# Kernel optimization log

Measured on AMD Instinct MI355X. Metric: run time of the kernel, lower is better.

## Reference

```python
import jax, jax.numpy as jnp
import numpy as np

N_NODES = 100000
N_EDGES = 3200000
NODE_DIM = 16      # output_size_node
EDGE_IN = 2 * NODE_DIM  # input_size_Edge = 32
EDGE_OUT = 9
HIDDEN = 9
MSG_ROUNDS = 3


def _mlp_params(key, d_in, d_hid, d_out):
    k1, k2, k3 = jax.random.split(key, 3)
    s1 = 1.0 / np.sqrt(d_in)
    s2 = 1.0 / np.sqrt(d_hid)
    return (
        jax.random.normal(k1, (d_in, d_hid), jnp.float32) * s1,
        jnp.zeros((d_hid,), jnp.float32),
        jax.random.normal(k2, (d_hid, d_hid), jnp.float32) * s2,
        jnp.zeros((d_hid,), jnp.float32),
        jax.random.normal(k3, (d_hid, d_out), jnp.float32) * s2,
        jnp.zeros((d_out,), jnp.float32),
    )


def setup_inputs() -> dict:
    key = jax.random.key(0)
    kx, ks, kd, kfe, kfx = jax.random.split(key, 5)
    X = jax.random.normal(kx, (N_NODES, NODE_DIM), jnp.float32)
    edge_src = jax.random.randint(ks, (N_EDGES,), 0, N_NODES, jnp.int32)
    edge_dst = jax.random.randint(kd, (N_EDGES,), 0, N_NODES, jnp.int32)
    fe = _mlp_params(kfe, EDGE_IN, HIDDEN, EDGE_OUT)
    fx = _mlp_params(kfx, EDGE_OUT + NODE_DIM, HIDDEN, NODE_DIM)
    return {
        "X": X, "edge_src": edge_src, "edge_dst": edge_dst,
        "fe_W1": fe[0], "fe_b1": fe[1], "fe_W2": fe[2], "fe_b2": fe[3], "fe_W3": fe[4], "fe_b3": fe[5],
        "fx_W1": fx[0], "fx_b1": fx[1], "fx_W2": fx[2], "fx_b2": fx[3], "fx_W3": fx[4], "fx_b3": fx[5],
    }


def _mlp3(h, W1, b1, W2, b2, W3, b3):
    # 3-layer MLP with relu hidden activations (MLP_nonlinear, act='relu')
    h = jax.nn.relu(h @ W1 + b1)
    h = jax.nn.relu(h @ W2 + b2)
    return h @ W3 + b3


def reference(X, edge_src, edge_dst,
              fe_W1, fe_b1, fe_W2, fe_b2, fe_W3, fe_b3,
              fx_W1, fx_b1, fx_W2, fx_b2, fx_W3, fx_b3):
    n = X.shape[0]
    for _ in range(MSG_ROUNDS):
        # per-edge message: fe(cat(X[i], X[j])) with i=receiver(dst), j=sender(src)
        e_in = jnp.concatenate([X[edge_dst], X[edge_src]], axis=-1)  # [E, 2*D]
        msgs = _mlp3(e_in, fe_W1, fe_b1, fe_W2, fe_b2, fe_W3, fe_b3)  # [E, 9]
        m = jax.ops.segment_sum(msgs, edge_dst, num_segments=n)       # [N, 9]
        # per-node update: fx(cat(X[i], m_i))
        X = _mlp3(jnp.concatenate([X, m], axis=-1),
                  fx_W1, fx_b1, fx_W2, fx_b2, fx_W3, fx_b3)           # [N, D]
    return X
```

## Files before the change

### kernel.cpp

```cpp
#include <hip/hip_runtime.h>


constexpr int NN = 100000;
constexpr int NE = 3200000;
constexpr int NBK = (NN + 127) / 128;
constexpr int SLOT = 8192;
constexpr int EPB = 4096;
constexpr int NBLK_SORT = (NE + EPB - 1) / EPB;
constexpr int NB_NODE = (NN + 255) / 256;


__global__ __launch_bounds__(256) void bsort_k(const int* __restrict__ src,
                                               const int* __restrict__ dst,
                                               int* __restrict__ gcursor,
                                               unsigned* __restrict__ sed)
{
    __shared__ int lhist[NBK];
    __shared__ int lbase[NBK];
    const int t = threadIdx.x;
    for (int i = t; i < NBK; i += 256) lhist[i] = 0;
    __syncthreads();

    const int blkbase = blockIdx.x * EPB;
    unsigned pr[16], sv[16];
    #pragma unroll
    for (int k = 0; k < 16; ++k) {
        const int e = blkbase + k * 256 + t;
        if (e < NE) {
            const int d = dst[e];
            const int s = src[e];
            const int bin = d >> 7;
            const int r = atomicAdd(&lhist[bin], 1);
            pr[k] = ((unsigned)bin << 13) | (unsigned)r;
            sv[k] = ((unsigned)(d & 127) << 17) | (unsigned)s;
        } else {
            pr[k] = 0xFFFFFFFFu;
        }
    }
    __syncthreads();

    for (int i = t; i < NBK; i += 256) {
        const int c = lhist[i];
        if (c) lbase[i] = atomicAdd(&gcursor[i], c);
    }
    __syncthreads();

    #pragma unroll
    for (int k = 0; k < 16; ++k) {
        if (pr[k] != 0xFFFFFFFFu) {
            const int bin = (int)(pr[k] >> 13);
            const int r = (int)(pr[k] & 0x1FFFu);
            sed[(size_t)bin * SLOT + lbase[bin] + r] = sv[k];
        }
    }
}


__global__ __launch_bounds__(512) void lsort_k(unsigned* __restrict__ sed,
                                               const int* __restrict__ gcursor)
{
    __shared__ unsigned buf[SLOT];
    __shared__ unsigned obuf[SLOT];
    __shared__ int hist[128];
    __shared__ int cur[128];
    const int t = threadIdx.x;
    const int b = blockIdx.x;
    const int base = b * SLOT;
    int fill = gcursor[b];
    if (fill > SLOT) fill = SLOT;

    if (t < 128) hist[t] = 0;
    __syncthreads();
    for (int i = t; i < fill; i += 512) {
        unsigned v = sed[base + i];
        buf[i] = v;
        atomicAdd(&hist[v >> 17], 1);
    }
    __syncthreads();
    if (t < 128) cur[t] = hist[t];
    __syncthreads();
    for (int off = 1; off < 128; off <<= 1) {
        int a = (t < 128 && t >= off) ? cur[t - off] : 0;
        __syncthreads();
        if (t < 128) cur[t] += a;
        __syncthreads();
    }
    if (t < 128) cur[t] -= hist[t];
    __syncthreads();
    for (int i = t; i < fill; i += 512) {
        unsigned v = buf[i];
        int r = atomicAdd(&cur[v >> 17], 1);
        obuf[r] = v;
    }
    __syncthreads();
    for (int i = t; i < fill; i += 512) sed[base + i] = obuf[i];
}


__global__ __launch_bounds__(256) void base_k(const float* __restrict__ X,
                                              const float* __restrict__ feW1,
                                              const float* __restrict__ feb1,
                                              float* __restrict__ base1,
                                              float* __restrict__ bases,
                                              float* __restrict__ m)
{
    const int n = blockIdx.x * 256 + threadIdx.x;
    if (n >= NN) return;

    float x[16];
    const float4* p = reinterpret_cast<const float4*>(X + (size_t)n * 16);
    #pragma unroll
    for (int q = 0; q < 4; ++q) {
        float4 v = p[q];
        x[4*q] = v.x; x[4*q+1] = v.y; x[4*q+2] = v.z; x[4*q+3] = v.w;
    }
    float bd[9];
    #pragma unroll
    for (int j = 0; j < 9; ++j) bd[j] = feb1[j];
    #pragma unroll
    for (int i = 0; i < 16; ++i) {
        const float xi = x[i];
        #pragma unroll
        for (int j = 0; j < 9; ++j) bd[j] = fmaf(xi, feW1[i * 9 + j], bd[j]);
    }
    float bs[9];
    #pragma unroll
    for (int j = 0; j < 9; ++j) bs[j] = 0.f;
    #pragma unroll
    for (int i = 0; i < 16; ++i) {
        const float xi = x[i];
        #pragma unroll
        for (int j = 0; j < 9; ++j) bs[j] = fmaf(xi, feW1[(16 + i) * 9 + j], bs[j]);
    }
    float* bp = base1 + (size_t)n * 12;
    #pragma unroll
    for (int j = 0; j < 9; ++j) bp[j] = bd[j];
    float* sp = bases + (size_t)n * 16;
    #pragma unroll
    for (int j = 0; j < 9; ++j) sp[j] = bs[j];
    float* mp = m + (size_t)n * 10;
    #pragma unroll
    for (int j = 0; j < 10; ++j) mp[j] = 0.f;
}


__global__ __launch_bounds__(256) void edge9_k(
    const float* __restrict__ base1,
    const float* __restrict__ bases,
    const unsigned* __restrict__ sed,
    const int* __restrict__ gcursor,
    const float* __restrict__ feW2, const float* __restrict__ feb2,
    float* __restrict__ m)
{
    const int t = threadIdx.x;
    const int b = blockIdx.x >> 5;
    const int idx0 = (blockIdx.x & 31) * 256;
    const int fill = gcursor[b];
    if (idx0 >= fill) return;

    const int idx = idx0 + t;
    const bool valid = idx < fill;
    const int lane = t & 63;
    const int cidx = valid ? idx : fill - 1;
    const unsigned pk = sed[(size_t)b * SLOT + cidx];
    const int dla = (int)(pk >> 17);
    const int s   = (int)(pk & 0x1FFFFu);
    const int dl  = valid ? dla : 128 + lane;

    float a[9];
    {
        const float4* pb = reinterpret_cast<const float4*>(base1 + (size_t)(b * 128 + dla) * 12);
        float4 b0 = pb[0], b1 = pb[1];
        const float b8 = base1[(size_t)(b * 128 + dla) * 12 + 8];
        const float4* ps = reinterpret_cast<const float4*>(bases + (size_t)s * 16);
        float4 c0 = ps[0], c1 = ps[1];
        const float c8 = bases[(size_t)s * 16 + 8];
        a[0] = b0.x + c0.x; a[1] = b0.y + c0.y; a[2] = b0.z + c0.z; a[3] = b0.w + c0.w;
        a[4] = b1.x + c1.x; a[5] = b1.y + c1.y; a[6] = b1.z + c1.z; a[7] = b1.w + c1.w;
        a[8] = b8 + c8;
    }
    #pragma unroll
    for (int j = 0; j < 9; ++j) a[j] = fmaxf(a[j], 0.f);

    float o[9];
    #pragma unroll
    for (int j = 0; j < 9; ++j) o[j] = feb2[j];
    #pragma unroll
    for (int i = 0; i < 9; ++i) {
        const float ai = a[i];
        #pragma unroll
        for (int j = 0; j < 9; ++j) o[j] = fmaf(ai, feW2[i * 9 + j], o[j]);
    }
    #pragma unroll
    for (int j = 0; j < 9; ++j) o[j] = fmaxf(o[j], 0.f);

    const int dprev = __shfl_up(dl, 1);
    const bool head = (lane == 0) || (dprev != dl);
    const unsigned long long hm = __ballot(head);
    const int dist = __clzll((long long)(hm << (63 - lane)));
    #pragma unroll
    for (int off = 1; off < 64; off <<= 1) {
        const bool ok = (dist >= off);
        #pragma unroll
        for (int j = 0; j < 9; ++j) {
            const float ov = __shfl_up(o[j], off);
            o[j] += ok ? ov : 0.f;
        }
    }
    const bool tail = (lane == 63) || (((hm >> (lane + 1)) & 1ull) != 0ull);
    if (tail && valid) {
        float* mp = m + (size_t)(b * 128 + dl) * 10;
        #pragma unroll
        for (int j = 0; j < 9; ++j) atomicAdd(mp + j, o[j]);
        atomicAdd(mp + 9, (float)(dist + 1));
    }
}


__global__ __launch_bounds__(256) void node8_k(
    const float* __restrict__ Xin, float* __restrict__ m,
    const float* __restrict__ fxW1, const float* __restrict__ fxb1,
    const float* __restrict__ fxW2, const float* __restrict__ fxb2,
    const float* __restrict__ fxW3, const float* __restrict__ fxb3,
    const float* __restrict__ feW1, const float* __restrict__ feb1,
    const float* __restrict__ feW3, const float* __restrict__ feb3,
    float* __restrict__ Xout, float* __restrict__ base1out,
    float* __restrict__ basesout)
{
    const int n = blockIdx.x * 256 + threadIdx.x;
    if (n >= NN) return;

    float xr[16];
    {
        const float4* p = reinterpret_cast<const float4*>(Xin + (size_t)n * 16);
        #pragma unroll
        for (int q = 0; q < 4; ++q) {
            float4 v = p[q];
            xr[4*q] = v.x; xr[4*q+1] = v.y; xr[4*q+2] = v.z; xr[4*q+3] = v.w;
        }
    }
    float S[9], deg;
    float* mp = m + (size_t)n * 10;
    #pragma unroll
    for (int j = 0; j < 9; ++j) S[j] = mp[j];
    deg = mp[9];
    #pragma unroll
    for (int j = 0; j < 10; ++j) mp[j] = 0.f;

    float mm[9];
    #pragma unroll
    for (int j = 0; j < 9; ++j) mm[j] = deg * feb3[j];
    #pragma unroll
    for (int i = 0; i < 9; ++i) {
        const float si = S[i];
        #pragma unroll
        for (int j = 0; j < 9; ++j) mm[j] = fmaf(si, feW3[i * 9 + j], mm[j]);
    }

    float h1[9];
    #pragma unroll
    for (int j = 0; j < 9; ++j) h1[j] = fxb1[j];
    #pragma unroll
    for (int i = 0; i < 16; ++i) {
        const float xi = xr[i];
        #pragma unroll
        for (int j = 0; j < 9; ++j) h1[j] = fmaf(xi, fxW1[i * 9 + j], h1[j]);
    }
    #pragma unroll
    for (int i = 0; i < 9; ++i) {
        const float xi = mm[i];
        #pragma unroll
        for (int j = 0; j < 9; ++j) h1[j] = fmaf(xi, fxW1[(16 + i) * 9 + j], h1[j]);
    }
    #pragma unroll
    for (int j = 0; j < 9; ++j) h1[j] = fmaxf(h1[j], 0.f);

    float h2[9];
    #pragma unroll
    for (int j = 0; j < 9; ++j) h2[j] = fxb2[j];
    #pragma unroll
    for (int i = 0; i < 9; ++i) {
        const float xi = h1[i];
        #pragma unroll
        for (int j = 0; j < 9; ++j) h2[j] = fmaf(xi, fxW2[i * 9 + j], h2[j]);
    }
    #pragma unroll
    for (int j = 0; j < 9; ++j) h2[j] = fmaxf(h2[j], 0.f);

    float o[16];
    #pragma unroll
    for (int k = 0; k < 16; ++k) o[k] = fxb3[k];
    #pragma unroll
    for (int j = 0; j < 9; ++j) {
        const float hj = h2[j];
        #pragma unroll
        for (int k = 0; k < 16; ++k) o[k] = fmaf(hj, fxW3[j * 16 + k], o[k]);
    }

    float4* po = reinterpret_cast<float4*>(Xout + (size_t)n * 16);
    #pragma unroll
    for (int q = 0; q < 4; ++q) {
        float4 v;
        v.x = o[4*q]; v.y = o[4*q+1]; v.z = o[4*q+2]; v.w = o[4*q+3];
        po[q] = v;
    }

    float bb[9];
    #pragma unroll
    for (int j = 0; j < 9; ++j) bb[j] = feb1[j];
    #pragma unroll
    for (int i = 0; i < 16; ++i) {
        const float xi = o[i];
        #pragma unroll
        for (int j = 0; j < 9; ++j) bb[j] = fmaf(xi, feW1[i * 9 + j], bb[j]);
    }
    float* bp = base1out + (size_t)n * 12;
    #pragma unroll
    for (int j = 0; j < 9; ++j) bp[j] = bb[j];

    float cc[9];
    #pragma unroll
    for (int j = 0; j < 9; ++j) cc[j] = 0.f;
    #pragma unroll
    for (int i = 0; i < 16; ++i) {
        const float xi = o[i];
        #pragma unroll
        for (int j = 0; j < 9; ++j) cc[j] = fmaf(xi, feW1[(16 + i) * 9 + j], cc[j]);
    }
    float* sp = basesout + (size_t)n * 16;
    #pragma unroll
    for (int j = 0; j < 9; ++j) sp[j] = cc[j];
}

extern "C" void kernel_launch(void* const* d_in, const int* in_sizes, int n_in,
                              void* d_out, int out_size, void* d_ws, size_t ws_size,
                              hipStream_t stream)
{
    (void)in_sizes; (void)n_in; (void)out_size; (void)ws_size;
    const float* X0   = (const float*)d_in[0];
    const int*   esrc = (const int*)d_in[1];
    const int*   edst = (const int*)d_in[2];
    const float* feW1 = (const float*)d_in[3];
    const float* feb1 = (const float*)d_in[4];
    const float* feW2 = (const float*)d_in[5];
    const float* feb2 = (const float*)d_in[6];
    const float* feW3 = (const float*)d_in[7];
    const float* feb3 = (const float*)d_in[8];
    const float* fxW1 = (const float*)d_in[9];
    const float* fxb1 = (const float*)d_in[10];
    const float* fxW2 = (const float*)d_in[11];
    const float* fxb2 = (const float*)d_in[12];
    const float* fxW3 = (const float*)d_in[13];
    const float* fxb3 = (const float*)d_in[14];
    float* out = (float*)d_out;

    float* base1  = (float*)d_ws;
    float* bases  = base1 + (size_t)NN * 12;
    float* mb     = bases + (size_t)NN * 16;
    int* gcursor  = (int*)(mb + (size_t)NN * 10);
    unsigned* sed = (unsigned*)(gcursor + 1024);

    const dim3 thr(256);
    const dim3 gS(NBLK_SORT);
    const dim3 gL(NBK);
    const dim3 gE(NBK * (SLOT / 256));
    const dim3 gN(NB_NODE);

    hipMemsetAsync(gcursor, 0, NBK * sizeof(int), stream);
    bsort_k<<<gS, thr, 0, stream>>>(esrc, edst, gcursor, sed);
    lsort_k<<<gL, dim3(512), 0, stream>>>(sed, gcursor);

    base_k<<<gN, thr, 0, stream>>>(X0, feW1, feb1, base1, bases, mb);
    edge9_k<<<gE, thr, 0, stream>>>(base1, bases, sed, gcursor, feW2, feb2, mb);
    node8_k<<<gN, thr, 0, stream>>>(X0, mb, fxW1, fxb1, fxW2, fxb2, fxW3, fxb3,
                                    feW1, feb1, feW3, feb3, out, base1, bases);
    edge9_k<<<gE, thr, 0, stream>>>(base1, bases, sed, gcursor, feW2, feb2, mb);
    node8_k<<<gN, thr, 0, stream>>>(out, mb, fxW1, fxb1, fxW2, fxb2, fxW3, fxb3,
                                    feW1, feb1, feW3, feb3, out, base1, bases);
    edge9_k<<<gE, thr, 0, stream>>>(base1, bases, sed, gcursor, feW2, feb2, mb);
    node8_k<<<gN, thr, 0, stream>>>(out, mb, fxW1, fxb1, fxW2, fxb2, fxW3, fxb3,
                                    feW1, feb1, feW3, feb3, out, base1, bases);
}
```

Measured before the change: 492.4 us.

## Process two sorted edges per thread in edge kernel with paired segmented scan

The edge kernel now has each thread handle two consecutive sorted edges, loaded as one uint2. The two messages are pre-combined when they share a destination, and a single segmented warp scan runs over the pairs, with the count carried as a tenth channel. This halves the number of threads and the shuffle-scan work per edge and widens the index loads, at the cost of more registers per thread and more complex head/tail atomic logic. Out-of-range source indices are clamped so padding slots can be read safely.

```diff
diff --git a/kernel.cpp b/kernel.cpp
--- a/kernel.cpp
+++ b/kernel.cpp
@@ -144,7 +144,7 @@
 }
 
 
-__global__ __launch_bounds__(256) void edge9_k(
+__global__ __launch_bounds__(256) void edge11_k(
     const float* __restrict__ base1,
     const float* __restrict__ bases,
     const unsigned* __restrict__ sed,
@@ -153,66 +153,114 @@
     float* __restrict__ m)
 {
     const int t = threadIdx.x;
-    const int b = blockIdx.x >> 5;
-    const int idx0 = (blockIdx.x & 31) * 256;
+    const int b = blockIdx.x >> 4;
+    const int idx0 = (blockIdx.x & 15) * 512;
     const int fill = gcursor[b];
     if (idx0 >= fill) return;
 
-    const int idx = idx0 + t;
-    const bool valid = idx < fill;
     const int lane = t & 63;
-    const int cidx = valid ? idx : fill - 1;
-    const unsigned pk = sed[(size_t)b * SLOT + cidx];
-    const int dla = (int)(pk >> 17);
-    const int s   = (int)(pk & 0x1FFFFu);
-    const int dl  = valid ? dla : 128 + lane;
-
-    float a[9];
+    const int start = idx0 + (t >> 6) * 128;
+    if (start >= fill) return;
+
+    const int e0 = start + 2 * lane;
+    const bool v0 = e0 < fill;
+    const bool v1 = e0 + 1 < fill;
+
+    const uint2 pk = *reinterpret_cast<const uint2*>(sed + (size_t)b * SLOT + e0);
+    const int d0 = (int)(pk.x >> 17);
+    const int d1 = (int)(pk.y >> 17);
+    int s0 = (int)(pk.x & 0x1FFFFu);  s0 = s0 < NN ? s0 : NN - 1;
+    int s1 = (int)(pk.y & 0x1FFFFu);  s1 = s1 < NN ? s1 : NN - 1;
+    const int k0 = v0 ? d0 : (160 + 2 * lane);
+    const int k1 = v1 ? d1 : (161 + 2 * lane);
+
+    float o0[9], o1[9];
     {
-        const float4* pb = reinterpret_cast<const float4*>(base1 + (size_t)(b * 128 + dla) * 12);
+        const float4* pb = reinterpret_cast<const float4*>(base1 + (size_t)(b * 128 + d0) * 12);
         float4 b0 = pb[0], b1 = pb[1];
-        const float b8 = base1[(size_t)(b * 128 + dla) * 12 + 8];
-        const float4* ps = reinterpret_cast<const float4*>(bases + (size_t)s * 16);
+        const float b8 = base1[(size_t)(b * 128 + d0) * 12 + 8];
+        const float4* ps = reinterpret_cast<const float4*>(bases + (size_t)s0 * 16);
         float4 c0 = ps[0], c1 = ps[1];
-        const float c8 = bases[(size_t)s * 16 + 8];
+        const float c8 = bases[(size_t)s0 * 16 + 8];
+        float a[9];
         a[0] = b0.x + c0.x; a[1] = b0.y + c0.y; a[2] = b0.z + c0.z; a[3] = b0.w + c0.w;
         a[4] = b1.x + c1.x; a[5] = b1.y + c1.y; a[6] = b1.z + c1.z; a[7] = b1.w + c1.w;
         a[8] = b8 + c8;
-    }
-    #pragma unroll
-    for (int j = 0; j < 9; ++j) a[j] = fmaxf(a[j], 0.f);
-
-    float o[9];
-    #pragma unroll
-    for (int j = 0; j < 9; ++j) o[j] = feb2[j];
-    #pragma unroll
-    for (int i = 0; i < 9; ++i) {
-        const float ai = a[i];
-        #pragma unroll
-        for (int j = 0; j < 9; ++j) o[j] = fmaf(ai, feW2[i * 9 + j], o[j]);
-    }
-    #pragma unroll
-    for (int j = 0; j < 9; ++j) o[j] = fmaxf(o[j], 0.f);
-
-    const int dprev = __shfl_up(dl, 1);
-    const bool head = (lane == 0) || (dprev != dl);
+        #pragma unroll
+        for (int j = 0; j < 9; ++j) a[j] = fmaxf(a[j], 0.f);
+        #pragma unroll
+        for (int j = 0; j < 9; ++j) o0[j] = feb2[j];
+        #pragma unroll
+        for (int i = 0; i < 9; ++i) {
+            const float ai = a[i];
+            #pragma unroll
+            for (int j = 0; j < 9; ++j) o0[j] = fmaf(ai, feW2[i * 9 + j], o0[j]);
+        }
+        #pragma unroll
+        for (int j = 0; j < 9; ++j) o0[j] = fmaxf(o0[j], 0.f);
+    }
+    {
+        const float4* pb = reinterpret_cast<const float4*>(base1 + (size_t)(b * 128 + d1) * 12);
+        float4 b0 = pb[0], b1 = pb[1];
+        const float b8 = base1[(size_t)(b * 128 + d1) * 12 + 8];
+        const float4* ps = reinterpret_cast<const float4*>(bases + (size_t)s1 * 16);
+        float4 c0 = ps[0], c1 = ps[1];
+        const float c8 = bases[(size_t)s1 * 16 + 8];
+        float a[9];
+        a[0] = b0.x + c0.x; a[1] = b0.y + c0.y; a[2] = b0.z + c0.z; a[3] = b0.w + c0.w;
+        a[4] = b1.x + c1.x; a[5] = b1.y + c1.y; a[6] = b1.z + c1.z; a[7] = b1.w + c1.w;
+        a[8] = b8 + c8;
+        #pragma unroll
+        for (int j = 0; j < 9; ++j) a[j] = fmaxf(a[j], 0.f);
+        #pragma unroll
+        for (int j = 0; j < 9; ++j) o1[j] = feb2[j];
+        #pragma unroll
+        for (int i = 0; i < 9; ++i) {
+            const float ai = a[i];
+            #pragma unroll
+            for (int j = 0; j < 9; ++j) o1[j] = fmaf(ai, feW2[i * 9 + j], o1[j]);
+        }
+        #pragma unroll
+        for (int j = 0; j < 9; ++j) o1[j] = fmaxf(o1[j], 0.f);
+    }
+
+    const bool same = (k0 == k1);
+    float S[10];
+    #pragma unroll
+    for (int j = 0; j < 9; ++j) S[j] = same ? (o0[j] + o1[j]) : o1[j];
+    S[9] = same ? 2.f : (v1 ? 1.f : 0.f);
+
+    const int pkey = __shfl_up(k1, 1);
+    const bool head = (lane == 0) || (pkey != k1);
     const unsigned long long hm = __ballot(head);
     const int dist = __clzll((long long)(hm << (63 - lane)));
     #pragma unroll
     for (int off = 1; off < 64; off <<= 1) {
         const bool ok = (dist >= off);
         #pragma unroll
-        for (int j = 0; j < 9; ++j) {
-            const float ov = __shfl_up(o[j], off);
-            o[j] += ok ? ov : 0.f;
-        }
-    }
-    const bool tail = (lane == 63) || (((hm >> (lane + 1)) & 1ull) != 0ull);
-    if (tail && valid) {
-        float* mp = m + (size_t)(b * 128 + dl) * 10;
-        #pragma unroll
-        for (int j = 0; j < 9; ++j) atomicAdd(mp + j, o[j]);
-        atomicAdd(mp + 9, (float)(dist + 1));
+        for (int j = 0; j < 10; ++j) {
+            const float ov = __shfl_up(S[j], off);
+            S[j] += ok ? ov : 0.f;
+        }
+    }
+    float P[10];
+    #pragma unroll
+    for (int j = 0; j < 10; ++j) P[j] = __shfl_up(S[j], 1);
+
+    if (!same && v0) {
+        const bool link = (lane > 0) && (pkey == k0);
+        float* mp = m + (size_t)(b * 128 + d0) * 10;
+        #pragma unroll
+        for (int j = 0; j < 9; ++j) atomicAdd(mp + j, (link ? P[j] : 0.f) + o0[j]);
+        atomicAdd(mp + 9, (link ? P[9] : 0.f) + 1.f);
+    }
+    const int nk0 = __shfl_down(k0, 1);
+    const bool tail = v1 && ((lane == 63) || (nk0 != k1));
+    if (tail) {
+        float* mp = m + (size_t)(b * 128 + d1) * 10;
+        #pragma unroll
+        for (int j = 0; j < 9; ++j) atomicAdd(mp + j, S[j]);
+        atomicAdd(mp + 9, S[9]);
     }
 }
 
@@ -363,7 +411,7 @@
     const dim3 thr(256);
     const dim3 gS(NBLK_SORT);
     const dim3 gL(NBK);
-    const dim3 gE(NBK * (SLOT / 256));
+    const dim3 gE(NBK * (SLOT / 512));
     const dim3 gN(NB_NODE);
 
     hipMemsetAsync(gcursor, 0, NBK * sizeof(int), stream);
@@ -371,13 +419,13 @@
     lsort_k<<<gL, dim3(512), 0, stream>>>(sed, gcursor);
 
     base_k<<<gN, thr, 0, stream>>>(X0, feW1, feb1, base1, bases, mb);
-    edge9_k<<<gE, thr, 0, stream>>>(base1, bases, sed, gcursor, feW2, feb2, mb);
+    edge11_k<<<gE, thr, 0, stream>>>(base1, bases, sed, gcursor, feW2, feb2, mb);
     node8_k<<<gN, thr, 0, stream>>>(X0, mb, fxW1, fxb1, fxW2, fxb2, fxW3, fxb3,
                                     feW1, feb1, feW3, feb3, out, base1, bases);
-    edge9_k<<<gE, thr, 0, stream>>>(base1, bases, sed, gcursor, feW2, feb2, mb);
+    edge11_k<<<gE, thr, 0, stream>>>(base1, bases, sed, gcursor, feW2, feb2, mb);
     node8_k<<<gN, thr, 0, stream>>>(out, mb, fxW1, fxb1, fxW2, fxb2, fxW3, fxb3,
                                     feW1, feb1, feW3, feb3, out, base1, bases);
-    edge9_k<<<gE, thr, 0, stream>>>(base1, bases, sed, gcursor, feW2, feb2, mb);
+    edge11_k<<<gE, thr, 0, stream>>>(base1, bases, sed, gcursor, feW2, feb2, mb);
     node8_k<<<gN, thr, 0, stream>>>(out, mb, fxW1, fxb1, fxW2, fxb2, fxW3, fxb3,
                                     feW1, feb1, feW3, feb3, out, base1, bases);
 }
```

New measurement: 550.3 us. 1.12x slower.
